# Kernel optimization log

Hardware: AMD Instinct MI355X
Metric: run time of the kernel (lower is better)

## Reference

```python
import jax, jax.numpy as jnp
import numpy as np

H = 128      # hidden_channels
FN = 6       # in_channels_node
FE = 3       # in_channels_edge
N = 40000    # nodes per chunk (pointnum)
E = 240000   # edges
C = 2        # per_t * batch_size chunks
S = 4        # n_mp_down[0] message-passing steps


def _ln(x, g, b, eps=1e-5):
    m = jnp.mean(x, axis=-1, keepdims=True)
    v = jnp.mean((x - m) ** 2, axis=-1, keepdims=True)
    return (x - m) * jax.lax.rsqrt(v + eps) * g + b


def setup_inputs() -> dict:
    key = jax.random.key(0)
    ks = iter(jax.random.split(key, 64))
    def W(*shape):
        fan_in = shape[-2]
        return jax.random.normal(next(ks), shape, jnp.float32) * (1.0 / np.sqrt(fan_in))
    z = lambda *s: jnp.zeros(s, jnp.float32)
    o = lambda *s: jnp.ones(s, jnp.float32)
    inp = {
        "x": jax.random.normal(next(ks), (C * N, FN), jnp.float32),
        "edge_attr": jax.random.normal(next(ks), (E, FE), jnp.float32),
        "mean_vec_x": jax.random.normal(next(ks), (FN,), jnp.float32) * 0.1,
        "std_vec_x": o(FN),
        "mean_vec_edge": jax.random.normal(next(ks), (FE,), jnp.float32) * 0.1,
        "std_vec_edge": o(FE),
        # node encoder: 3 linears + LayerNorm
        "nenc_w0": W(FN, H), "nenc_b0": z(H),
        "nenc_w1": W(H, H), "nenc_b1": z(H),
        "nenc_w2": W(H, H), "nenc_b2": z(H),
        "nenc_g": o(H), "nenc_be": z(H),
        # edge encoder: 3 linears + LayerNorm
        "eenc_w0": W(FE, H), "eenc_b0": z(H),
        "eenc_w1": W(H, H), "eenc_b1": z(H),
        "eenc_w2": W(H, H), "eenc_b2": z(H),
        "eenc_g": o(H), "eenc_be": z(H),
        # per-step edge MLPs (n_mlp_mp=2), stacked over S steps
        "emp_w0": W(S, 3 * H, H), "emp_b0": z(S, H),
        "emp_w1": W(S, H, H), "emp_b1": z(S, H),
        "emp_g": o(S, H), "emp_be": z(S, H),
        # per-step node MLPs
        "nmp_w0": W(S, 2 * H, H), "nmp_b0": z(S, H),
        "nmp_w1": W(S, H, H), "nmp_b1": z(S, H),
        "nmp_g": o(S, H), "nmp_be": z(S, H),
        "edge_index": jax.random.randint(next(ks), (2, E), 0, N, jnp.int32),
        "per_t": 2,
        "batch_size": 1,
    }
    return inp


def _forward(x, edge_attr, mean_vec_x, std_vec_x, mean_vec_edge, std_vec_edge,
             nenc_w0, nenc_b0, nenc_w1, nenc_b1, nenc_w2, nenc_b2, nenc_g, nenc_be,
             eenc_w0, eenc_b0, eenc_w1, eenc_b1, eenc_w2, eenc_b2, eenc_g, eenc_be,
             emp_w0, emp_b0, emp_w1, emp_b1, emp_g, emp_be,
             nmp_w0, nmp_b0, nmp_w1, nmp_b1, nmp_g, nmp_be,
             edge_index, per_t, batch_size):
    act = jax.nn.elu
    ei0, ei1 = edge_index[0], edge_index[1]
    chunks = per_t * batch_size
    n = x.shape[0] // chunks  # pointnum
    # edge encoding is identical for every chunk (shared edge_attr)
    e = (edge_attr - mean_vec_edge) / std_vec_edge
    e = act(e @ eenc_w0 + eenc_b0)
    e = act(e @ eenc_w1 + eenc_b1)
    e = e @ eenc_w2 + eenc_b2
    e0 = _ln(e, eenc_g, eenc_be)
    # scatter-mean denominator (PyG aggr='mean' at target nodes ei1)
    cnt = jax.ops.segment_sum(jnp.ones((ei1.shape[0], 1), x.dtype), ei1, num_segments=n)
    cnt = jnp.maximum(cnt, 1.0)

    def chunk(xc):  # xc: [n, FN]
        h = (xc - mean_vec_x) / std_vec_x
        h = act(h @ nenc_w0 + nenc_b0)
        h = act(h @ nenc_w1 + nenc_b1)
        h = h @ nenc_w2 + nenc_b2
        h = _ln(h, nenc_g, nenc_be)
        e = e0
        for s in range(S):
            # per-edge: gather -> concat -> 2-layer MLP -> residual -> LN
            et = jnp.concatenate([h[ei0], h[ei1], e], axis=-1)  # [E, 3H]
            et = act(et @ emp_w0[s] + emp_b0[s]) @ emp_w1[s] + emp_b1[s]
            e = _ln(e + et, emp_g[s], emp_be[s])
            # scatter-mean of edge features to target nodes
            agg = jax.ops.segment_sum(e, ei1, num_segments=n) / cnt  # [n, H]
            # per-node: concat -> 2-layer MLP -> residual -> LN
            ht = jnp.concatenate([h, agg], axis=-1)  # [n, 2H]
            ht = act(ht @ nmp_w0[s] + nmp_b0[s]) @ nmp_w1[s] + nmp_b1[s]
            h = _ln(h + ht, nmp_g[s], nmp_be[s])
        return h

    return jax.vmap(chunk)(x.reshape(chunks, n, FN))  # [C, n, H]


def reference(x, edge_attr, mean_vec_x, std_vec_x, mean_vec_edge, std_vec_edge,
              nenc_w0, nenc_b0, nenc_w1, nenc_b1, nenc_w2, nenc_b2, nenc_g, nenc_be,
              eenc_w0, eenc_b0, eenc_w1, eenc_b1, eenc_w2, eenc_b2, eenc_g, eenc_be,
              emp_w0, emp_b0, emp_w1, emp_b1, emp_g, emp_be,
              nmp_w0, nmp_b0, nmp_w1, nmp_b1, nmp_g, nmp_be,
              edge_index, per_t, batch_size):
    return _forward(x, edge_attr, mean_vec_x, std_vec_x, mean_vec_edge, std_vec_edge,
                    nenc_w0, nenc_b0, nenc_w1, nenc_b1, nenc_w2, nenc_b2, nenc_g, nenc_be,
                    eenc_w0, eenc_b0, eenc_w1, eenc_b1, eenc_w2, eenc_b2, eenc_g, eenc_be,
                    emp_w0, emp_b0, emp_w1, emp_b1, emp_g, emp_be,
                    nmp_w0, nmp_b0, nmp_w1, nmp_b1, nmp_g, nmp_be,
                    edge_index, per_t, batch_size)
```

## Files before the change

kernel.cpp:

```cpp
#include <hip/hip_runtime.h>
#include <math.h>

constexpr int HD  = 128;
constexpr int FNN = 6;
constexpr int FEE = 3;
constexpr int NN  = 40000;
constexpr int EE  = 240000;
constexpr int SS  = 4;

typedef __bf16 bf16_t;
typedef bf16_t bf16x8 __attribute__((ext_vector_type(8)));
typedef float  f32x4  __attribute__((ext_vector_type(4)));

__device__ __forceinline__ f32x4 mfma16(bf16x8 a, bf16x8 b, f32x4 c){
  return __builtin_amdgcn_mfma_f32_16x16x32_bf16(a, b, c, 0, 0, 0);
}
__device__ __forceinline__ float elu(float v){ return v > 0.f ? v : __expf(v) - 1.f; }

struct PackJob { const float* src; int K; };
struct PackArgs { PackJob j[30]; };

__global__ void __launch_bounds__(256) k_pack(PackArgs pa, bf16_t* __restrict__ dst){
  int gid = blockIdx.x*256 + threadIdx.x;
  int base = 0;
  #pragma unroll 1
  for (int i = 0; i < 30; ++i){
    int Kp = (pa.j[i].K + 31) & ~31;
    int sz = Kp * HD;
    if (gid < base + sz){
      int idx = gid - base;
      int jj = idx & 7, c = (idx >> 3) & 127, G = idx >> 10;
      int k = G*8 + jj;
      float v = (k < pa.j[i].K) ? pa.j[i].src[(size_t)k*HD + c] : 0.f;
      dst[base + idx] = (bf16_t)v;
      return;
    }
    base += sz;
  }
}

__global__ void k_cnt(const int* __restrict__ ei1, int* __restrict__ cnt){
  int t = blockIdx.x*blockDim.x + threadIdx.x;
  if (t < EE) atomicAdd(cnt + ei1[t], 1);
}

__global__ void __launch_bounds__(1024) k_scanA(const int* __restrict__ cnt,
    int* __restrict__ incl, int* __restrict__ bsum){
  __shared__ int sd[1024];
  int i = blockIdx.x*1024 + (int)threadIdx.x;
  int v = (i < NN) ? cnt[i] : 0;
  sd[threadIdx.x] = v;
  __syncthreads();
  #pragma unroll
  for (int ofs = 1; ofs < 1024; ofs <<= 1){
    int t = (threadIdx.x >= (unsigned)ofs) ? sd[threadIdx.x - ofs] : 0;
    __syncthreads();
    sd[threadIdx.x] += t;
    __syncthreads();
  }
  if (i < NN) incl[i] = sd[threadIdx.x];
  if (threadIdx.x == 1023) bsum[blockIdx.x] = sd[1023];
}
__global__ void k_scanB(const int* __restrict__ bsum, int* __restrict__ boff, int nb){
  if (threadIdx.x == 0){
    int acc = 0;
    for (int b = 0; b < nb; ++b){ boff[b] = acc; acc += bsum[b]; }
    boff[nb] = acc;
  }
}
__global__ void __launch_bounds__(1024) k_scanC(const int* __restrict__ cnt,
    const int* __restrict__ incl, const int* __restrict__ boff,
    int* __restrict__ rowstart, int* __restrict__ cursor, float* __restrict__ inv){
  int i = blockIdx.x*1024 + (int)threadIdx.x;
  if (i < NN){
    int c = cnt[i];
    int start = boff[blockIdx.x] + incl[i] - c;
    rowstart[i] = start;
    cursor[i]   = start;
    inv[i] = 1.f / fmaxf((float)c, 1.f);
  }
  if (blockIdx.x == 0 && threadIdx.x == 0) rowstart[NN] = boff[gridDim.x];
}

__global__ void k_fill(const int* __restrict__ ei0, const int* __restrict__ ei1,
                       int* __restrict__ cursor, int* __restrict__ perm,
                       int2* __restrict__ eidx2){
  int t = blockIdx.x*blockDim.x + threadIdx.x;
  if (t < EE){
    int n1 = ei1[t];
    int pos = atomicAdd(cursor + n1, 1);
    perm[pos] = t;
    int2 v; v.x = ei0[t]; v.y = n1;
    eidx2[pos] = v;
  }
}

__global__ void __launch_bounds__(256) k_agg(const bf16_t* __restrict__ e,
    const int* __restrict__ rowstart, const float* __restrict__ inv,
    bf16_t* __restrict__ agg){
  int gid = blockIdx.x*256 + (int)threadIdx.x;
  int node = gid >> 4, li = gid & 15;
  if (node >= NN) return;
  int s = rowstart[node], t = rowstart[node+1];
  float a[8] = {0,0,0,0,0,0,0,0};
  for (int ed = s; ed < t; ++ed){
    bf16x8 v = *(const bf16x8*)(e + (size_t)ed*HD + li*8);
    #pragma unroll
    for (int i = 0; i < 8; ++i) a[i] += (float)v[i];
  }
  float sc = inv[node];
  bf16x8 o;
  #pragma unroll
  for (int i = 0; i < 8; ++i) o[i] = (bf16_t)(a[i]*sc);
  *(bf16x8*)(agg + (size_t)node*HD + li*8) = o;
}

template<int FIN, bool ISNODE>
__global__ void __launch_bounds__(256) k_encoder(
    const float* __restrict__ xin, const float* __restrict__ mv, const float* __restrict__ sv,
    const float* __restrict__ w0,  const float* __restrict__ b0,
    const bf16_t* __restrict__ W1p, const float* __restrict__ b1,
    const bf16_t* __restrict__ W2p, const float* __restrict__ b2,
    const float* __restrict__ gg,  const float* __restrict__ bb,
    float* __restrict__ outf, bf16_t* __restrict__ outb,
    const int* __restrict__ perm)
{
  __shared__ bf16_t z0s[4][16][136];
  __shared__ bf16_t z1s[4][16][136];
  const int tid = threadIdx.x;
  const int w = tid >> 6, l = tid & 63, r = l & 15, grp = l >> 4;
  const int rowbase = blockIdx.x*64 + w*16;
  const int row = rowbase + r;
  const int src = perm ? perm[row] : row;

  float xn[FIN];
  #pragma unroll
  for (int f = 0; f < FIN; ++f) xn[f] = (xin[(size_t)src*FIN + f] - mv[f]) / sv[f];
  #pragma unroll
  for (int q = 0; q < 32; ++q){
    int c = grp*32 + q;
    float a = b0[c];
    #pragma unroll
    for (int f = 0; f < FIN; ++f) a += xn[f] * w0[f*HD + c];
    z0s[w][r][c] = (bf16_t)elu(a);
  }
  __syncthreads();

  bf16x8 a1[4];
  #pragma unroll
  for (int kt = 0; kt < 4; ++kt) a1[kt] = *(const bf16x8*)&z0s[w][r][kt*32 + grp*8];
  #pragma unroll
  for (int nt = 0; nt < 8; ++nt){
    int c = nt*16 + r;
    float bv = b1[c];
    f32x4 acc = {bv, bv, bv, bv};
    #pragma unroll
    for (int kt = 0; kt < 4; ++kt){
      bf16x8 bfr = *(const bf16x8*)(W1p + ((kt*4 + grp)*HD + c)*8);
      acc = mfma16(a1[kt], bfr, acc);
    }
    #pragma unroll
    for (int i = 0; i < 4; ++i) z1s[w][grp*4 + i][c] = (bf16_t)elu(acc[i]);
  }
  __syncthreads();

  bf16x8 a2[4];
  #pragma unroll
  for (int kt = 0; kt < 4; ++kt) a2[kt] = *(const bf16x8*)&z1s[w][r][kt*32 + grp*8];
  f32x4 et[8];
  #pragma unroll
  for (int nt = 0; nt < 8; ++nt){
    int c = nt*16 + r;
    float bv = b2[c];
    f32x4 acc = {bv, bv, bv, bv};
    #pragma unroll
    for (int kt = 0; kt < 4; ++kt){
      bf16x8 bfr = *(const bf16x8*)(W2p + ((kt*4 + grp)*HD + c)*8);
      acc = mfma16(a2[kt], bfr, acc);
    }
    et[nt] = acc;
  }

  f32x4 s = {0,0,0,0}, sq = {0,0,0,0};
  #pragma unroll
  for (int nt = 0; nt < 8; ++nt)
    #pragma unroll
    for (int i = 0; i < 4; ++i){ float v = et[nt][i]; s[i] += v; sq[i] += v*v; }
  #pragma unroll
  for (int m = 1; m < 16; m <<= 1)
    #pragma unroll
    for (int i = 0; i < 4; ++i){ s[i] += __shfl_xor(s[i], m, 64); sq[i] += __shfl_xor(sq[i], m, 64); }
  f32x4 mean, rstd;
  #pragma unroll
  for (int i = 0; i < 4; ++i){
    float mu = s[i] * (1.f/HD);
    float va = sq[i] * (1.f/HD) - mu*mu;
    mean[i] = mu; rstd[i] = rsqrtf(va + 1e-5f);
  }
  #pragma unroll
  for (int nt = 0; nt < 8; ++nt){
    int c = nt*16 + r;
    float gv = gg[c], bv = bb[c];
    #pragma unroll
    for (int i = 0; i < 4; ++i){
      float o = (et[nt][i] - mean[i]) * rstd[i] * gv + bv;
      size_t oidx = (size_t)(rowbase + grp*4 + i)*HD + c;
      outb[oidx] = (bf16_t)o;
      if constexpr (ISNODE) outf[oidx] = o;
    }
  }
}

__global__ void __launch_bounds__(256) k_hpartial(
    const bf16_t* __restrict__ hbf,
    const bf16_t* __restrict__ Wap, const bf16_t* __restrict__ Wbp,
    bf16_t* __restrict__ p0, bf16_t* __restrict__ p1)
{
  const int tid = threadIdx.x;
  const int w = tid >> 6, l = tid & 63, r = l & 15, grp = l >> 4;
  const int rowbase = blockIdx.x*64 + w*16;
  const int row = rowbase + r;

  bf16x8 afr[4];
  #pragma unroll
  for (int kt = 0; kt < 4; ++kt)
    afr[kt] = *(const bf16x8*)(hbf + (size_t)row*HD + kt*32 + grp*8);

  #pragma unroll
  for (int nt = 0; nt < 8; ++nt){
    int c = nt*16 + r;
    f32x4 a0 = {0,0,0,0}, a1 = {0,0,0,0};
    #pragma unroll
    for (int kt = 0; kt < 4; ++kt){
      bf16x8 bfa = *(const bf16x8*)(Wap + ((kt*4 + grp)*HD + c)*8);
      bf16x8 bfb = *(const bf16x8*)(Wbp + ((kt*4 + grp)*HD + c)*8);
      a0 = mfma16(afr[kt], bfa, a0);
      a1 = mfma16(afr[kt], bfb, a1);
    }
    #pragma unroll
    for (int i = 0; i < 4; ++i){
      size_t oidx = (size_t)(rowbase + grp*4 + i)*HD + c;
      p0[oidx] = (bf16_t)a0[i];
      p1[oidx] = (bf16_t)a1[i];
    }
  }
}

__global__ void __launch_bounds__(256) k_edge_mlp(
    const bf16_t* __restrict__ p0g, const bf16_t* __restrict__ p1g,
    const bf16_t* e_in, bf16_t* e_out,
    const bf16_t* __restrict__ W0ep, const float* __restrict__ b0,
    const bf16_t* __restrict__ W1p, const float* __restrict__ b1,
    const float* __restrict__ gg,  const float* __restrict__ bb,
    const int2* __restrict__ eidx2)
{
  __shared__ bf16_t z1s_all[4][16][136];
  const int tid = threadIdx.x;
  const int w = tid >> 6, l = tid & 63, r = l & 15, grp = l >> 4;
  const int rowbase = blockIdx.x*64 + w*16;
  const int row = rowbase + r;
  bf16_t (*z1)[136] = z1s_all[w];

  {
    const int sr = l >> 2, cq = (l & 3)*32;
    const int2 nnS = eidx2[rowbase + sr];
    const bf16_t* P0 = p0g + (size_t)nnS.x*HD + cq;
    const bf16_t* P1 = p1g + (size_t)nnS.y*HD + cq;
    #pragma unroll
    for (int q = 0; q < 4; ++q){
      bf16x8 u = *(const bf16x8*)(P0 + q*8);
      bf16x8 v = *(const bf16x8*)(P1 + q*8);
      bf16x8 sm;
      #pragma unroll
      for (int i = 0; i < 8; ++i) sm[i] = (bf16_t)((float)u[i] + (float)v[i]);
      *(bf16x8*)&z1[sr][cq + q*8] = sm;
    }
  }

  bf16x8 afr[4];
  #pragma unroll
  for (int kt = 0; kt < 4; ++kt)
    afr[kt] = *(const bf16x8*)(e_in + (size_t)row*HD + kt*32 + grp*8);
  __builtin_amdgcn_wave_barrier();

  #pragma unroll
  for (int nt = 0; nt < 8; ++nt){
    int c = nt*16 + r;
    float bv = b0[c];
    f32x4 acc = {bv, bv, bv, bv};
    #pragma unroll
    for (int kt = 0; kt < 4; ++kt){
      bf16x8 bfr = *(const bf16x8*)(W0ep + ((kt*4 + grp)*HD + c)*8);
      acc = mfma16(afr[kt], bfr, acc);
    }
    #pragma unroll
    for (int i = 0; i < 4; ++i){
      float pv = (float)z1[grp*4 + i][c];
      z1[grp*4 + i][c] = (bf16_t)elu(acc[i] + pv);
    }
  }
  __builtin_amdgcn_wave_barrier();

  bf16x8 a2[4];
  #pragma unroll
  for (int kt = 0; kt < 4; ++kt) a2[kt] = *(const bf16x8*)&z1[r][kt*32 + grp*8];
  f32x4 et[8];
  #pragma unroll
  for (int nt = 0; nt < 8; ++nt){
    int c = nt*16 + r;
    float bv = b1[c];
    f32x4 acc = {bv, bv, bv, bv};
    #pragma unroll
    for (int kt = 0; kt < 4; ++kt){
      bf16x8 bfr = *(const bf16x8*)(W1p + ((kt*4 + grp)*HD + c)*8);
      acc = mfma16(a2[kt], bfr, acc);
    }
    et[nt] = acc;
  }

  f32x4 s = {0,0,0,0}, sq = {0,0,0,0};
  #pragma unroll
  for (int nt = 0; nt < 8; ++nt){
    int c = nt*16 + r;
    #pragma unroll
    for (int i = 0; i < 4; ++i){
      float v = et[nt][i] + (float)e_in[(size_t)(rowbase + grp*4 + i)*HD + c];
      et[nt][i] = v; s[i] += v; sq[i] += v*v;
    }
  }
  #pragma unroll
  for (int m = 1; m < 16; m <<= 1)
    #pragma unroll
    for (int i = 0; i < 4; ++i){ s[i] += __shfl_xor(s[i], m, 64); sq[i] += __shfl_xor(sq[i], m, 64); }
  f32x4 mean, rstd;
  #pragma unroll
  for (int i = 0; i < 4; ++i){
    float mu = s[i] * (1.f/HD);
    float va = sq[i] * (1.f/HD) - mu*mu;
    mean[i] = mu; rstd[i] = rsqrtf(va + 1e-5f);
  }
  #pragma unroll
  for (int nt = 0; nt < 8; ++nt){
    int c = nt*16 + r;
    float gv = gg[c], bv = bb[c];
    #pragma unroll
    for (int i = 0; i < 4; ++i)
      e_out[(size_t)(rowbase + grp*4 + i)*HD + c] =
          (bf16_t)((et[nt][i] - mean[i]) * rstd[i] * gv + bv);
  }
}

template<bool DOPART>
__global__ void __launch_bounds__(256) k_node_mlp(
    bf16_t* hbf, const bf16_t* __restrict__ agg,
    const bf16_t* __restrict__ W0p, const float* __restrict__ b0,
    const bf16_t* __restrict__ W1p, const float* __restrict__ b1,
    const float* __restrict__ gg,  const float* __restrict__ bb,
    float* hout,
    const bf16_t* __restrict__ Wap, const bf16_t* __restrict__ Wbp,
    bf16_t* __restrict__ p0, bf16_t* __restrict__ p1)
{
  __shared__ bf16_t z1s[4][16][136];
  const int tid = threadIdx.x;
  const int w = tid >> 6, l = tid & 63, r = l & 15, grp = l >> 4;
  const int rowbase = blockIdx.x*64 + w*16;
  const int row = rowbase + r;

  bf16x8 afr[8];
  #pragma unroll
  for (int kt = 0; kt < 4; ++kt)
    afr[kt] = *(const bf16x8*)(hbf + (size_t)row*HD + kt*32 + grp*8);
  #pragma unroll
  for (int kt = 0; kt < 4; ++kt)
    afr[4+kt] = *(const bf16x8*)(agg + (size_t)row*HD + kt*32 + grp*8);

  #pragma unroll
  for (int nt = 0; nt < 8; ++nt){
    int c = nt*16 + r;
    float bv = b0[c];
    f32x4 acc = {bv, bv, bv, bv};
    #pragma unroll
    for (int kt = 0; kt < 8; ++kt){
      bf16x8 bfr = *(const bf16x8*)(W0p + ((kt*4 + grp)*HD + c)*8);
      acc = mfma16(afr[kt], bfr, acc);
    }
    #pragma unroll
    for (int i = 0; i < 4; ++i) z1s[w][grp*4 + i][c] = (bf16_t)elu(acc[i]);
  }
  __syncthreads();

  bf16x8 a2[4];
  #pragma unroll
  for (int kt = 0; kt < 4; ++kt) a2[kt] = *(const bf16x8*)&z1s[w][r][kt*32 + grp*8];
  f32x4 et[8];
  #pragma unroll
  for (int nt = 0; nt < 8; ++nt){
    int c = nt*16 + r;
    float bv = b1[c];
    f32x4 acc = {bv, bv, bv, bv};
    #pragma unroll
    for (int kt = 0; kt < 4; ++kt){
      bf16x8 bfr = *(const bf16x8*)(W1p + ((kt*4 + grp)*HD + c)*8);
      acc = mfma16(a2[kt], bfr, acc);
    }
    et[nt] = acc;
  }

  f32x4 s = {0,0,0,0}, sq = {0,0,0,0};
  #pragma unroll
  for (int nt = 0; nt < 8; ++nt){
    int c = nt*16 + r;
    #pragma unroll
    for (int i = 0; i < 4; ++i){
      float v = et[nt][i] + hout[(size_t)(rowbase + grp*4 + i)*HD + c];
      et[nt][i] = v; s[i] += v; sq[i] += v*v;
    }
  }
  #pragma unroll
  for (int m = 1; m < 16; m <<= 1)
    #pragma unroll
    for (int i = 0; i < 4; ++i){ s[i] += __shfl_xor(s[i], m, 64); sq[i] += __shfl_xor(sq[i], m, 64); }
  f32x4 mean, rstd;
  #pragma unroll
  for (int i = 0; i < 4; ++i){
    float mu = s[i] * (1.f/HD);
    float va = sq[i] * (1.f/HD) - mu*mu;
    mean[i] = mu; rstd[i] = rsqrtf(va + 1e-5f);
  }
  #pragma unroll
  for (int nt = 0; nt < 8; ++nt){
    int c = nt*16 + r;
    float gv = gg[c], bv = bb[c];
    #pragma unroll
    for (int i = 0; i < 4; ++i){
      float o = (et[nt][i] - mean[i]) * rstd[i] * gv + bv;
      size_t oidx = (size_t)(rowbase + grp*4 + i)*HD + c;
      bf16_t ob = (bf16_t)o;
      hout[oidx] = o;
      hbf[oidx]  = ob;
      if constexpr (DOPART) z1s[w][grp*4 + i][c] = ob;
    }
  }

  if constexpr (DOPART){
    __builtin_amdgcn_wave_barrier();
    bf16x8 ah[4];
    #pragma unroll
    for (int kt = 0; kt < 4; ++kt) ah[kt] = *(const bf16x8*)&z1s[w][r][kt*32 + grp*8];
    #pragma unroll
    for (int nt = 0; nt < 8; ++nt){
      int c = nt*16 + r;
      f32x4 a0 = {0,0,0,0}, a1 = {0,0,0,0};
      #pragma unroll
      for (int kt = 0; kt < 4; ++kt){
        bf16x8 bfa = *(const bf16x8*)(Wap + ((kt*4 + grp)*HD + c)*8);
        bf16x8 bfb = *(const bf16x8*)(Wbp + ((kt*4 + grp)*HD + c)*8);
        a0 = mfma16(ah[kt], bfa, a0);
        a1 = mfma16(ah[kt], bfb, a1);
      }
      #pragma unroll
      for (int i = 0; i < 4; ++i){
        size_t oidx = (size_t)(rowbase + grp*4 + i)*HD + c;
        p0[oidx] = (bf16_t)a0[i];
        p1[oidx] = (bf16_t)a1[i];
      }
    }
  }
}

extern "C" void kernel_launch(void* const* d_in, const int* in_sizes, int n_in,
                              void* d_out, int out_size, void* d_ws, size_t ws_size,
                              hipStream_t stream)
{
  (void)in_sizes; (void)n_in; (void)out_size; (void)ws_size;
  const float* x         = (const float*)d_in[0];
  const float* edge_attr = (const float*)d_in[1];
  const float* mvx = (const float*)d_in[2];
  const float* svx = (const float*)d_in[3];
  const float* mve = (const float*)d_in[4];
  const float* sve = (const float*)d_in[5];
  const float* nenc_w0 = (const float*)d_in[6];
  const float* nenc_b0 = (const float*)d_in[7];
  const float* nenc_w1 = (const float*)d_in[8];
  const float* nenc_b1 = (const float*)d_in[9];
  const float* nenc_w2 = (const float*)d_in[10];
  const float* nenc_b2 = (const float*)d_in[11];
  const float* nenc_g  = (const float*)d_in[12];
  const float* nenc_be = (const float*)d_in[13];
  const float* eenc_w0 = (const float*)d_in[14];
  const float* eenc_b0 = (const float*)d_in[15];
  const float* eenc_w1 = (const float*)d_in[16];
  const float* eenc_b1 = (const float*)d_in[17];
  const float* eenc_w2 = (const float*)d_in[18];
  const float* eenc_b2 = (const float*)d_in[19];
  const float* eenc_g  = (const float*)d_in[20];
  const float* eenc_be = (const float*)d_in[21];
  const float* emp_w0 = (const float*)d_in[22];
  const float* emp_b0 = (const float*)d_in[23];
  const float* emp_w1 = (const float*)d_in[24];
  const float* emp_b1 = (const float*)d_in[25];
  const float* emp_g  = (const float*)d_in[26];
  const float* emp_be = (const float*)d_in[27];
  const float* nmp_w0 = (const float*)d_in[28];
  const float* nmp_b0 = (const float*)d_in[29];
  const float* nmp_w1 = (const float*)d_in[30];
  const float* nmp_b1 = (const float*)d_in[31];
  const float* nmp_g  = (const float*)d_in[32];
  const float* nmp_be = (const float*)d_in[33];
  const int* eidx = (const int*)d_in[34];
  const int* ei0 = eidx;
  const int* ei1 = eidx + EE;
  float* out = (float*)d_out;

  char* ws = (char*)d_ws;
  size_t off = 0;
  bf16_t* e_cur = (bf16_t*)(ws + off); off += (size_t)EE*HD*2;
  bf16_t* e0    = (bf16_t*)(ws + off); off += (size_t)EE*HD*2;
  bf16_t* hbf   = (bf16_t*)(ws + off); off += (size_t)NN*HD*2;
  bf16_t* agg   = (bf16_t*)(ws + off); size_t agg_off = off; off += (size_t)NN*HD*2;
  bf16_t* p0    = (bf16_t*)(ws + off); off += (size_t)NN*HD*2;
  bf16_t* p1    = (bf16_t*)(ws + off); off += (size_t)NN*HD*2;
  float*  inv   = (float*)(ws + off);  off += (size_t)NN*4;
  int*    rowst = (int*)(ws + off);    off += (size_t)(NN+1)*4 + 12;
  int*    perm  = (int*)(ws + off);    off += (size_t)EE*4;
  int2*   eidx2 = (int2*)(ws + off);   off += (size_t)EE*8;
  bf16_t* wpk   = (bf16_t*)(ws + off);
  int*    cnt_i = (int*)(ws + agg_off);
  int*    curs  = (int*)(ws + agg_off + (size_t)NN*4);
  int*    incl  = (int*)(ws + agg_off + (size_t)2*NN*4);
  int*    bsum  = (int*)(ws + agg_off + (size_t)3*NN*4);
  int*    boff  = (int*)(ws + agg_off + (size_t)3*NN*4 + 256);

  const int NB = (NN + 1023)/1024;

  hipMemsetAsync(cnt_i, 0, NN*sizeof(int), stream);
  k_cnt<<<(EE + 255)/256, 256, 0, stream>>>(ei1, cnt_i);
  k_scanA<<<NB, 1024, 0, stream>>>(cnt_i, incl, bsum);
  k_scanB<<<1, 64, 0, stream>>>(bsum, boff, NB);
  k_scanC<<<NB, 1024, 0, stream>>>(cnt_i, incl, boff, rowst, curs, inv);
  k_fill<<<(EE + 255)/256, 256, 0, stream>>>(ei0, ei1, curs, perm, eidx2);

  PackArgs pa;
  const float* srcs[30] = {
    eenc_w0, eenc_w1, eenc_w2, nenc_w0, nenc_w1, nenc_w2,
    emp_w0,           emp_w0 + 49152,           emp_w0 + 2*49152,           emp_w0 + 3*49152,
    emp_w0 + 16384,   emp_w0 + 49152 + 16384,   emp_w0 + 2*49152 + 16384,   emp_w0 + 3*49152 + 16384,
    emp_w0 + 32768,   emp_w0 + 49152 + 32768,   emp_w0 + 2*49152 + 32768,   emp_w0 + 3*49152 + 32768,
    emp_w1, emp_w1 + 16384, emp_w1 + 2*16384, emp_w1 + 3*16384,
    nmp_w0, nmp_w0 + 32768, nmp_w0 + 2*32768, nmp_w0 + 3*32768,
    nmp_w1, nmp_w1 + 16384, nmp_w1 + 2*16384, nmp_w1 + 3*16384 };
  const int KsA[30] = {FEE,128,128,FNN,128,128,
                       128,128,128,128, 128,128,128,128, 128,128,128,128,
                       128,128,128,128, 256,256,256,256, 128,128,128,128};
  int offs[30]; int tot = 0;
  for (int i = 0; i < 30; ++i){
    pa.j[i].src = srcs[i]; pa.j[i].K = KsA[i];
    offs[i] = tot; tot += ((KsA[i] + 31) & ~31) * HD;
  }
  k_pack<<<(tot + 255)/256, 256, 0, stream>>>(pa, wpk);

  k_encoder<FEE,false><<<EE/64, 256, 0, stream>>>(edge_attr, mve, sve,
      eenc_w0, eenc_b0, wpk + offs[1], eenc_b1, wpk + offs[2], eenc_b2,
      eenc_g, eenc_be, nullptr, e0, perm);

  for (int c = 0; c < 2; ++c){
    float* hout = out + (size_t)c*NN*HD;
    k_encoder<FNN,true><<<NN/64, 256, 0, stream>>>(x + (size_t)c*NN*FNN, mvx, svx,
        nenc_w0, nenc_b0, wpk + offs[4], nenc_b1, wpk + offs[5], nenc_b2,
        nenc_g, nenc_be, hout, hbf, nullptr);
    k_hpartial<<<NN/64, 256, 0, stream>>>(hbf, wpk + offs[6], wpk + offs[10], p0, p1);
    for (int s = 0; s < SS; ++s){
      const bf16_t* e_in = (s == 0) ? e0 : e_cur;
      k_edge_mlp<<<EE/64, 256, 0, stream>>>(p0, p1, e_in, e_cur,
          wpk + offs[14+s], emp_b0 + s*HD, wpk + offs[18+s], emp_b1 + s*HD,
          emp_g + s*HD, emp_be + s*HD, eidx2);
      k_agg<<<(NN*16 + 255)/256, 256, 0, stream>>>(e_cur, rowst, inv, agg);
      if (s < SS-1){
        k_node_mlp<true><<<NN/64, 256, 0, stream>>>(hbf, agg,
            wpk + offs[22+s], nmp_b0 + s*HD, wpk + offs[26+s], nmp_b1 + s*HD,
            nmp_g + s*HD, nmp_be + s*HD, hout,
            wpk + offs[6+(s+1)], wpk + offs[10+(s+1)], p0, p1);
      } else {
        k_node_mlp<false><<<NN/64, 256, 0, stream>>>(hbf, agg,
            wpk + offs[22+s], nmp_b0 + s*HD, wpk + offs[26+s], nmp_b1 + s*HD,
            nmp_g + s*HD, nmp_be + s*HD, hout,
            nullptr, nullptr, nullptr, nullptr);
      }
    }
  }
}
```

Measured before the change: 1.082 ms.

## Batch both graph chunks into single launches per stage

```diff
diff --git a/kernel.cpp b/kernel.cpp
--- a/kernel.cpp
+++ b/kernel.cpp
@@ -7,6 +7,8 @@
 constexpr int NN  = 40000;
 constexpr int EE  = 240000;
 constexpr int SS  = 4;
+constexpr size_t NHD = (size_t)NN*HD;
+constexpr size_t EHD = (size_t)EE*HD;
 
 typedef __bf16 bf16_t;
 typedef bf16_t bf16x8 __attribute__((ext_vector_type(8)));
@@ -97,8 +99,11 @@
 
 __global__ void __launch_bounds__(256) k_agg(const bf16_t* __restrict__ e,
     const int* __restrict__ rowstart, const float* __restrict__ inv,
-    bf16_t* __restrict__ agg){
-  int gid = blockIdx.x*256 + (int)threadIdx.x;
+    bf16_t* __restrict__ agg, int nblk){
+  int bid = blockIdx.x; int c = bid / nblk; int b = bid - c*nblk;
+  e   += (size_t)c*EHD;
+  agg += (size_t)c*NHD;
+  int gid = b*256 + (int)threadIdx.x;
   int node = gid >> 4, li = gid & 15;
   if (node >= NN) return;
   int s = rowstart[node], t = rowstart[node+1];
@@ -122,14 +127,20 @@
     const bf16_t* __restrict__ W1p, const float* __restrict__ b1,
     const bf16_t* __restrict__ W2p, const float* __restrict__ b2,
     const float* __restrict__ gg,  const float* __restrict__ bb,
-    float* __restrict__ outf, bf16_t* __restrict__ outb,
-    const int* __restrict__ perm)
+    float* __restrict__ outf, bf16_t* __restrict__ outb, bf16_t* __restrict__ outb2,
+    const int* __restrict__ perm, int nblk)
 {
   __shared__ bf16_t z0s[4][16][136];
   __shared__ bf16_t z1s[4][16][136];
+  const int bid = blockIdx.x; const int c = bid / nblk; const int b = bid - c*nblk;
+  if constexpr (ISNODE){
+    xin  += (size_t)c*NN*FIN;
+    outf += (size_t)c*NHD;
+    outb += (size_t)c*NHD;
+  }
   const int tid = threadIdx.x;
   const int w = tid >> 6, l = tid & 63, r = l & 15, grp = l >> 4;
-  const int rowbase = blockIdx.x*64 + w*16;
+  const int rowbase = b*64 + w*16;
   const int row = rowbase + r;
   const int src = perm ? perm[row] : row;
 
@@ -138,11 +149,11 @@
   for (int f = 0; f < FIN; ++f) xn[f] = (xin[(size_t)src*FIN + f] - mv[f]) / sv[f];
   #pragma unroll
   for (int q = 0; q < 32; ++q){
-    int c = grp*32 + q;
-    float a = b0[c];
-    #pragma unroll
-    for (int f = 0; f < FIN; ++f) a += xn[f] * w0[f*HD + c];
-    z0s[w][r][c] = (bf16_t)elu(a);
+    int cc = grp*32 + q;
+    float a = b0[cc];
+    #pragma unroll
+    for (int f = 0; f < FIN; ++f) a += xn[f] * w0[f*HD + cc];
+    z0s[w][r][cc] = (bf16_t)elu(a);
   }
   __syncthreads();
 
@@ -151,16 +162,16 @@
   for (int kt = 0; kt < 4; ++kt) a1[kt] = *(const bf16x8*)&z0s[w][r][kt*32 + grp*8];
   #pragma unroll
   for (int nt = 0; nt < 8; ++nt){
-    int c = nt*16 + r;
-    float bv = b1[c];
+    int cc = nt*16 + r;
+    float bv = b1[cc];
     f32x4 acc = {bv, bv, bv, bv};
     #pragma unroll
     for (int kt = 0; kt < 4; ++kt){
-      bf16x8 bfr = *(const bf16x8*)(W1p + ((kt*4 + grp)*HD + c)*8);
+      bf16x8 bfr = *(const bf16x8*)(W1p + ((kt*4 + grp)*HD + cc)*8);
       acc = mfma16(a1[kt], bfr, acc);
     }
     #pragma unroll
-    for (int i = 0; i < 4; ++i) z1s[w][grp*4 + i][c] = (bf16_t)elu(acc[i]);
+    for (int i = 0; i < 4; ++i) z1s[w][grp*4 + i][cc] = (bf16_t)elu(acc[i]);
   }
   __syncthreads();
 
@@ -170,12 +181,12 @@
   f32x4 et[8];
   #pragma unroll
   for (int nt = 0; nt < 8; ++nt){
-    int c = nt*16 + r;
-    float bv = b2[c];
+    int cc = nt*16 + r;
+    float bv = b2[cc];
     f32x4 acc = {bv, bv, bv, bv};
     #pragma unroll
     for (int kt = 0; kt < 4; ++kt){
-      bf16x8 bfr = *(const bf16x8*)(W2p + ((kt*4 + grp)*HD + c)*8);
+      bf16x8 bfr = *(const bf16x8*)(W2p + ((kt*4 + grp)*HD + cc)*8);
       acc = mfma16(a2[kt], bfr, acc);
     }
     et[nt] = acc;
@@ -199,13 +210,15 @@
   }
   #pragma unroll
   for (int nt = 0; nt < 8; ++nt){
-    int c = nt*16 + r;
-    float gv = gg[c], bv = bb[c];
+    int cc = nt*16 + r;
+    float gv = gg[cc], bv = bb[cc];
     #pragma unroll
     for (int i = 0; i < 4; ++i){
       float o = (et[nt][i] - mean[i]) * rstd[i] * gv + bv;
-      size_t oidx = (size_t)(rowbase + grp*4 + i)*HD + c;
-      outb[oidx] = (bf16_t)o;
+      size_t oidx = (size_t)(rowbase + grp*4 + i)*HD + cc;
+      bf16_t ob = (bf16_t)o;
+      outb[oidx] = ob;
+      if (outb2) outb2[oidx] = ob;
       if constexpr (ISNODE) outf[oidx] = o;
     }
   }
@@ -214,11 +227,13 @@
 __global__ void __launch_bounds__(256) k_hpartial(
     const bf16_t* __restrict__ hbf,
     const bf16_t* __restrict__ Wap, const bf16_t* __restrict__ Wbp,
-    bf16_t* __restrict__ p0, bf16_t* __restrict__ p1)
+    bf16_t* __restrict__ p0, bf16_t* __restrict__ p1, int nblk)
 {
+  const int bid = blockIdx.x; const int c = bid / nblk; const int b = bid - c*nblk;
+  hbf += (size_t)c*NHD; p0 += (size_t)c*NHD; p1 += (size_t)c*NHD;
   const int tid = threadIdx.x;
   const int w = tid >> 6, l = tid & 63, r = l & 15, grp = l >> 4;
-  const int rowbase = blockIdx.x*64 + w*16;
+  const int rowbase = b*64 + w*16;
   const int row = rowbase + r;
 
   bf16x8 afr[4];
@@ -228,18 +243,18 @@
 
   #pragma unroll
   for (int nt = 0; nt < 8; ++nt){
-    int c = nt*16 + r;
+    int cc = nt*16 + r;
     f32x4 a0 = {0,0,0,0}, a1 = {0,0,0,0};
     #pragma unroll
     for (int kt = 0; kt < 4; ++kt){
-      bf16x8 bfa = *(const bf16x8*)(Wap + ((kt*4 + grp)*HD + c)*8);
-      bf16x8 bfb = *(const bf16x8*)(Wbp + ((kt*4 + grp)*HD + c)*8);
+      bf16x8 bfa = *(const bf16x8*)(Wap + ((kt*4 + grp)*HD + cc)*8);
+      bf16x8 bfb = *(const bf16x8*)(Wbp + ((kt*4 + grp)*HD + cc)*8);
       a0 = mfma16(afr[kt], bfa, a0);
       a1 = mfma16(afr[kt], bfb, a1);
     }
     #pragma unroll
     for (int i = 0; i < 4; ++i){
-      size_t oidx = (size_t)(rowbase + grp*4 + i)*HD + c;
+      size_t oidx = (size_t)(rowbase + grp*4 + i)*HD + cc;
       p0[oidx] = (bf16_t)a0[i];
       p1[oidx] = (bf16_t)a1[i];
     }
@@ -252,12 +267,15 @@
     const bf16_t* __restrict__ W0ep, const float* __restrict__ b0,
     const bf16_t* __restrict__ W1p, const float* __restrict__ b1,
     const float* __restrict__ gg,  const float* __restrict__ bb,
-    const int2* __restrict__ eidx2)
+    const int2* __restrict__ eidx2, int nblk)
 {
   __shared__ bf16_t z1s_all[4][16][136];
+  const int bid = blockIdx.x; const int c = bid / nblk; const int b = bid - c*nblk;
+  p0g += (size_t)c*NHD; p1g += (size_t)c*NHD;
+  e_in += (size_t)c*EHD; e_out += (size_t)c*EHD;
   const int tid = threadIdx.x;
   const int w = tid >> 6, l = tid & 63, r = l & 15, grp = l >> 4;
-  const int rowbase = blockIdx.x*64 + w*16;
+  const int rowbase = b*64 + w*16;
   const int row = rowbase + r;
   bf16_t (*z1)[136] = z1s_all[w];
 
@@ -285,18 +303,18 @@
 
   #pragma unroll
   for (int nt = 0; nt < 8; ++nt){
-    int c = nt*16 + r;
-    float bv = b0[c];
+    int cc = nt*16 + r;
+    float bv = b0[cc];
     f32x4 acc = {bv, bv, bv, bv};
     #pragma unroll
     for (int kt = 0; kt < 4; ++kt){
-      bf16x8 bfr = *(const bf16x8*)(W0ep + ((kt*4 + grp)*HD + c)*8);
+      bf16x8 bfr = *(const bf16x8*)(W0ep + ((kt*4 + grp)*HD + cc)*8);
       acc = mfma16(afr[kt], bfr, acc);
     }
     #pragma unroll
     for (int i = 0; i < 4; ++i){
-      float pv = (float)z1[grp*4 + i][c];
-      z1[grp*4 + i][c] = (bf16_t)elu(acc[i] + pv);
+      float pv = (float)z1[grp*4 + i][cc];
+      z1[grp*4 + i][cc] = (bf16_t)elu(acc[i] + pv);
     }
   }
   __builtin_amdgcn_wave_barrier();
@@ -307,12 +325,12 @@
   f32x4 et[8];
   #pragma unroll
   for (int nt = 0; nt < 8; ++nt){
-    int c = nt*16 + r;
-    float bv = b1[c];
+    int cc = nt*16 + r;
+    float bv = b1[cc];
     f32x4 acc = {bv, bv, bv, bv};
     #pragma unroll
     for (int kt = 0; kt < 4; ++kt){
-      bf16x8 bfr = *(const bf16x8*)(W1p + ((kt*4 + grp)*HD + c)*8);
+      bf16x8 bfr = *(const bf16x8*)(W1p + ((kt*4 + grp)*HD + cc)*8);
       acc = mfma16(a2[kt], bfr, acc);
     }
     et[nt] = acc;
@@ -321,10 +339,10 @@
   f32x4 s = {0,0,0,0}, sq = {0,0,0,0};
   #pragma unroll
   for (int nt = 0; nt < 8; ++nt){
-    int c = nt*16 + r;
+    int cc = nt*16 + r;
     #pragma unroll
     for (int i = 0; i < 4; ++i){
-      float v = et[nt][i] + (float)e_in[(size_t)(rowbase + grp*4 + i)*HD + c];
+      float v = et[nt][i] + (float)e_in[(size_t)(rowbase + grp*4 + i)*HD + cc];
       et[nt][i] = v; s[i] += v; sq[i] += v*v;
     }
   }
@@ -341,11 +359,11 @@
   }
   #pragma unroll
   for (int nt = 0; nt < 8; ++nt){
-    int c = nt*16 + r;
-    float gv = gg[c], bv = bb[c];
+    int cc = nt*16 + r;
+    float gv = gg[cc], bv = bb[cc];
     #pragma unroll
     for (int i = 0; i < 4; ++i)
-      e_out[(size_t)(rowbase + grp*4 + i)*HD + c] =
+      e_out[(size_t)(rowbase + grp*4 + i)*HD + cc] =
           (bf16_t)((et[nt][i] - mean[i]) * rstd[i] * gv + bv);
   }
 }
@@ -358,12 +376,15 @@
     const float* __restrict__ gg,  const float* __restrict__ bb,
     float* hout,
     const bf16_t* __restrict__ Wap, const bf16_t* __restrict__ Wbp,
-    bf16_t* __restrict__ p0, bf16_t* __restrict__ p1)
+    bf16_t* __restrict__ p0, bf16_t* __restrict__ p1, int nblk)
 {
   __shared__ bf16_t z1s[4][16][136];
+  const int bid = blockIdx.x; const int c = bid / nblk; const int b = bid - c*nblk;
+  hbf += (size_t)c*NHD; agg += (size_t)c*NHD; hout += (size_t)c*NHD;
+  if constexpr (DOPART){ p0 += (size_t)c*NHD; p1 += (size_t)c*NHD; }
   const int tid = threadIdx.x;
   const int w = tid >> 6, l = tid & 63, r = l & 15, grp = l >> 4;
-  const int rowbase = blockIdx.x*64 + w*16;
+  const int rowbase = b*64 + w*16;
   const int row = rowbase + r;
 
   bf16x8 afr[8];
@@ -376,16 +397,16 @@
 
   #pragma unroll
   for (int nt = 0; nt < 8; ++nt){
-    int c = nt*16 + r;
-    float bv = b0[c];
+    int cc = nt*16 + r;
+    float bv = b0[cc];
     f32x4 acc = {bv, bv, bv, bv};
     #pragma unroll
     for (int kt = 0; kt < 8; ++kt){
-      bf16x8 bfr = *(const bf16x8*)(W0p + ((kt*4 + grp)*HD + c)*8);
+      bf16x8 bfr = *(const bf16x8*)(W0p + ((kt*4 + grp)*HD + cc)*8);
       acc = mfma16(afr[kt], bfr, acc);
     }
     #pragma unroll
-    for (int i = 0; i < 4; ++i) z1s[w][grp*4 + i][c] = (bf16_t)elu(acc[i]);
+    for (int i = 0; i < 4; ++i) z1s[w][grp*4 + i][cc] = (bf16_t)elu(acc[i]);
   }
   __syncthreads();
 
@@ -395,12 +416,12 @@
   f32x4 et[8];
   #pragma unroll
   for (int nt = 0; nt < 8; ++nt){
-    int c = nt*16 + r;
-    float bv = b1[c];
+    int cc = nt*16 + r;
+    float bv = b1[cc];
     f32x4 acc = {bv, bv, bv, bv};
     #pragma unroll
     for (int kt = 0; kt < 4; ++kt){
-      bf16x8 bfr = *(const bf16x8*)(W1p + ((kt*4 + grp)*HD + c)*8);
+      bf16x8 bfr = *(const bf16x8*)(W1p + ((kt*4 + grp)*HD + cc)*8);
       acc = mfma16(a2[kt], bfr, acc);
     }
     et[nt] = acc;
@@ -409,10 +430,10 @@
   f32x4 s = {0,0,0,0}, sq = {0,0,0,0};
   #pragma unroll
   for (int nt = 0; nt < 8; ++nt){
-    int c = nt*16 + r;
+    int cc = nt*16 + r;
     #pragma unroll
     for (int i = 0; i < 4; ++i){
-      float v = et[nt][i] + hout[(size_t)(rowbase + grp*4 + i)*HD + c];
+      float v = et[nt][i] + hout[(size_t)(rowbase + grp*4 + i)*HD + cc];
       et[nt][i] = v; s[i] += v; sq[i] += v*v;
     }
   }
@@ -429,16 +450,16 @@
   }
   #pragma unroll
   for (int nt = 0; nt < 8; ++nt){
-    int c = nt*16 + r;
-    float gv = gg[c], bv = bb[c];
+    int cc = nt*16 + r;
+    float gv = gg[cc], bv = bb[cc];
     #pragma unroll
     for (int i = 0; i < 4; ++i){
       float o = (et[nt][i] - mean[i]) * rstd[i] * gv + bv;
-      size_t oidx = (size_t)(rowbase + grp*4 + i)*HD + c;
+      size_t oidx = (size_t)(rowbase + grp*4 + i)*HD + cc;
       bf16_t ob = (bf16_t)o;
       hout[oidx] = o;
       hbf[oidx]  = ob;
-      if constexpr (DOPART) z1s[w][grp*4 + i][c] = ob;
+      if constexpr (DOPART) z1s[w][grp*4 + i][cc] = ob;
     }
   }
 
@@ -449,18 +470,18 @@
     for (int kt = 0; kt < 4; ++kt) ah[kt] = *(const bf16x8*)&z1s[w][r][kt*32 + grp*8];
     #pragma unroll
     for (int nt = 0; nt < 8; ++nt){
-      int c = nt*16 + r;
+      int cc = nt*16 + r;
       f32x4 a0 = {0,0,0,0}, a1 = {0,0,0,0};
       #pragma unroll
       for (int kt = 0; kt < 4; ++kt){
-        bf16x8 bfa = *(const bf16x8*)(Wap + ((kt*4 + grp)*HD + c)*8);
-        bf16x8 bfb = *(const bf16x8*)(Wbp + ((kt*4 + grp)*HD + c)*8);
+        bf16x8 bfa = *(const bf16x8*)(Wap + ((kt*4 + grp)*HD + cc)*8);
+        bf16x8 bfb = *(const bf16x8*)(Wbp + ((kt*4 + grp)*HD + cc)*8);
         a0 = mfma16(ah[kt], bfa, a0);
         a1 = mfma16(ah[kt], bfb, a1);
       }
       #pragma unroll
       for (int i = 0; i < 4; ++i){
-        size_t oidx = (size_t)(rowbase + grp*4 + i)*HD + c;
+        size_t oidx = (size_t)(rowbase + grp*4 + i)*HD + cc;
         p0[oidx] = (bf16_t)a0[i];
         p1[oidx] = (bf16_t)a1[i];
       }
@@ -472,7 +493,7 @@
                               void* d_out, int out_size, void* d_ws, size_t ws_size,
                               hipStream_t stream)
 {
-  (void)in_sizes; (void)n_in; (void)out_size; (void)ws_size;
+  (void)in_sizes; (void)n_in; (void)out_size;
   const float* x         = (const float*)d_in[0];
   const float* edge_attr = (const float*)d_in[1];
   const float* mvx = (const float*)d_in[2];
@@ -512,34 +533,6 @@
   const int* ei1 = eidx + EE;
   float* out = (float*)d_out;
 
-  char* ws = (char*)d_ws;
-  size_t off = 0;
-  bf16_t* e_cur = (bf16_t*)(ws + off); off += (size_t)EE*HD*2;
-  bf16_t* e0    = (bf16_t*)(ws + off); off += (size_t)EE*HD*2;
-  bf16_t* hbf   = (bf16_t*)(ws + off); off += (size_t)NN*HD*2;
-  bf16_t* agg   = (bf16_t*)(ws + off); size_t agg_off = off; off += (size_t)NN*HD*2;
-  bf16_t* p0    = (bf16_t*)(ws + off); off += (size_t)NN*HD*2;
-  bf16_t* p1    = (bf16_t*)(ws + off); off += (size_t)NN*HD*2;
-  float*  inv   = (float*)(ws + off);  off += (size_t)NN*4;
-  int*    rowst = (int*)(ws + off);    off += (size_t)(NN+1)*4 + 12;
-  int*    perm  = (int*)(ws + off);    off += (size_t)EE*4;
-  int2*   eidx2 = (int2*)(ws + off);   off += (size_t)EE*8;
-  bf16_t* wpk   = (bf16_t*)(ws + off);
-  int*    cnt_i = (int*)(ws + agg_off);
-  int*    curs  = (int*)(ws + agg_off + (size_t)NN*4);
-  int*    incl  = (int*)(ws + agg_off + (size_t)2*NN*4);
-  int*    bsum  = (int*)(ws + agg_off + (size_t)3*NN*4);
-  int*    boff  = (int*)(ws + agg_off + (size_t)3*NN*4 + 256);
-
-  const int NB = (NN + 1023)/1024;
-
-  hipMemsetAsync(cnt_i, 0, NN*sizeof(int), stream);
-  k_cnt<<<(EE + 255)/256, 256, 0, stream>>>(ei1, cnt_i);
-  k_scanA<<<NB, 1024, 0, stream>>>(cnt_i, incl, bsum);
-  k_scanB<<<1, 64, 0, stream>>>(bsum, boff, NB);
-  k_scanC<<<NB, 1024, 0, stream>>>(cnt_i, incl, boff, rowst, curs, inv);
-  k_fill<<<(EE + 255)/256, 256, 0, stream>>>(ei0, ei1, curs, perm, eidx2);
-
   PackArgs pa;
   const float* srcs[30] = {
     eenc_w0, eenc_w1, eenc_w2, nenc_w0, nenc_w1, nenc_w2,
@@ -557,35 +550,123 @@
     pa.j[i].src = srcs[i]; pa.j[i].K = KsA[i];
     offs[i] = tot; tot += ((KsA[i] + 31) & ~31) * HD;
   }
-  k_pack<<<(tot + 255)/256, 256, 0, stream>>>(pa, wpk);
-
-  k_encoder<FEE,false><<<EE/64, 256, 0, stream>>>(edge_attr, mve, sve,
-      eenc_w0, eenc_b0, wpk + offs[1], eenc_b1, wpk + offs[2], eenc_b2,
-      eenc_g, eenc_be, nullptr, e0, perm);
-
-  for (int c = 0; c < 2; ++c){
-    float* hout = out + (size_t)c*NN*HD;
-    k_encoder<FNN,true><<<NN/64, 256, 0, stream>>>(x + (size_t)c*NN*FNN, mvx, svx,
+
+  const int NBn = NN/64;
+  const int NBe = EE/64;
+  const int NBa = (NN*16 + 255)/256;
+  const int NB  = (NN + 1023)/1024;
+
+  size_t need_merged = 2*EHD*2 + 8*NHD*2 + (size_t)NN*4 + (size_t)(NN+1)*4 + 64
+                     + (size_t)EE*4 + (size_t)EE*8 + (size_t)tot*2 + 1024;
+
+  char* ws = (char*)d_ws;
+
+  if (ws_size >= need_merged){
+    size_t off = 0;
+    bf16_t* e_cur = (bf16_t*)(ws + off); off += 2*EHD*2;
+    bf16_t* hbf   = (bf16_t*)(ws + off); off += 2*NHD*2;
+    bf16_t* agg   = (bf16_t*)(ws + off); size_t agg_off = off; off += 2*NHD*2;
+    bf16_t* p0    = (bf16_t*)(ws + off); off += 2*NHD*2;
+    bf16_t* p1    = (bf16_t*)(ws + off); off += 2*NHD*2;
+    float*  inv   = (float*)(ws + off);  off += (size_t)NN*4;
+    int*    rowst = (int*)(ws + off);    off += (size_t)(NN+1)*4 + 12;
+    int*    perm  = (int*)(ws + off);    off += (size_t)EE*4;
+    int2*   eidx2 = (int2*)(ws + off);   off += (size_t)EE*8;
+    bf16_t* wpk   = (bf16_t*)(ws + off);
+    int*    cnt_i = (int*)(ws + agg_off);
+    int*    curs  = (int*)(ws + agg_off + (size_t)NN*4);
+    int*    incl  = (int*)(ws + agg_off + (size_t)2*NN*4);
+    int*    bsum  = (int*)(ws + agg_off + (size_t)3*NN*4);
+    int*    boff  = (int*)(ws + agg_off + (size_t)3*NN*4 + 256);
+
+    hipMemsetAsync(cnt_i, 0, NN*sizeof(int), stream);
+    k_cnt<<<(EE + 255)/256, 256, 0, stream>>>(ei1, cnt_i);
+    k_scanA<<<NB, 1024, 0, stream>>>(cnt_i, incl, bsum);
+    k_scanB<<<1, 64, 0, stream>>>(bsum, boff, NB);
+    k_scanC<<<NB, 1024, 0, stream>>>(cnt_i, incl, boff, rowst, curs, inv);
+    k_fill<<<(EE + 255)/256, 256, 0, stream>>>(ei0, ei1, curs, perm, eidx2);
+    k_pack<<<(tot + 255)/256, 256, 0, stream>>>(pa, wpk);
+
+    k_encoder<FEE,false><<<NBe, 256, 0, stream>>>(edge_attr, mve, sve,
+        eenc_w0, eenc_b0, wpk + offs[1], eenc_b1, wpk + offs[2], eenc_b2,
+        eenc_g, eenc_be, nullptr, e_cur, e_cur + EHD, perm, NBe);
+    k_encoder<FNN,true><<<2*NBn, 256, 0, stream>>>(x, mvx, svx,
         nenc_w0, nenc_b0, wpk + offs[4], nenc_b1, wpk + offs[5], nenc_b2,
-        nenc_g, nenc_be, hout, hbf, nullptr);
-    k_hpartial<<<NN/64, 256, 0, stream>>>(hbf, wpk + offs[6], wpk + offs[10], p0, p1);
+        nenc_g, nenc_be, out, hbf, nullptr, nullptr, NBn);
+    k_hpartial<<<2*NBn, 256, 0, stream>>>(hbf, wpk + offs[6], wpk + offs[10], p0, p1, NBn);
+
     for (int s = 0; s < SS; ++s){
-      const bf16_t* e_in = (s == 0) ? e0 : e_cur;
-      k_edge_mlp<<<EE/64, 256, 0, stream>>>(p0, p1, e_in, e_cur,
+      k_edge_mlp<<<2*NBe, 256, 0, stream>>>(p0, p1, e_cur, e_cur,
           wpk + offs[14+s], emp_b0 + s*HD, wpk + offs[18+s], emp_b1 + s*HD,
-          emp_g + s*HD, emp_be + s*HD, eidx2);
-      k_agg<<<(NN*16 + 255)/256, 256, 0, stream>>>(e_cur, rowst, inv, agg);
+          emp_g + s*HD, emp_be + s*HD, eidx2, NBe);
+      k_agg<<<2*NBa, 256, 0, stream>>>(e_cur, rowst, inv, agg, NBa);
       if (s < SS-1){
-        k_node_mlp<true><<<NN/64, 256, 0, stream>>>(hbf, agg,
+        k_node_mlp<true><<<2*NBn, 256, 0, stream>>>(hbf, agg,
             wpk + offs[22+s], nmp_b0 + s*HD, wpk + offs[26+s], nmp_b1 + s*HD,
-            nmp_g + s*HD, nmp_be + s*HD, hout,
-            wpk + offs[6+(s+1)], wpk + offs[10+(s+1)], p0, p1);
+            nmp_g + s*HD, nmp_be + s*HD, out,
+            wpk + offs[6+(s+1)], wpk + offs[10+(s+1)], p0, p1, NBn);
       } else {
-        k_node_mlp<false><<<NN/64, 256, 0, stream>>>(hbf, agg,
+        k_node_mlp<false><<<2*NBn, 256, 0, stream>>>(hbf, agg,
             wpk + offs[22+s], nmp_b0 + s*HD, wpk + offs[26+s], nmp_b1 + s*HD,
-            nmp_g + s*HD, nmp_be + s*HD, hout,
-            nullptr, nullptr, nullptr, nullptr);
+            nmp_g + s*HD, nmp_be + s*HD, out,
+            nullptr, nullptr, nullptr, nullptr, NBn);
       }
     }
-  }
-}
+  } else {
+    size_t off = 0;
+    bf16_t* e_cur = (bf16_t*)(ws + off); off += EHD*2;
+    bf16_t* e0    = (bf16_t*)(ws + off); off += EHD*2;
+    bf16_t* hbf   = (bf16_t*)(ws + off); off += NHD*2;
+    bf16_t* agg   = (bf16_t*)(ws + off); size_t agg_off = off; off += NHD*2;
+    bf16_t* p0    = (bf16_t*)(ws + off); off += NHD*2;
+    bf16_t* p1    = (bf16_t*)(ws + off); off += NHD*2;
+    float*  inv   = (float*)(ws + off);  off += (size_t)NN*4;
+    int*    rowst = (int*)(ws + off);    off += (size_t)(NN+1)*4 + 12;
+    int*    perm  = (int*)(ws + off);    off += (size_t)EE*4;
+    int2*   eidx2 = (int2*)(ws + off);   off += (size_t)EE*8;
+    bf16_t* wpk   = (bf16_t*)(ws + off);
+    int*    cnt_i = (int*)(ws + agg_off);
+    int*    curs  = (int*)(ws + agg_off + (size_t)NN*4);
+    int*    incl  = (int*)(ws + agg_off + (size_t)2*NN*4);
+    int*    bsum  = (int*)(ws + agg_off + (size_t)3*NN*4);
+    int*    boff  = (int*)(ws + agg_off + (size_t)3*NN*4 + 256);
+
+    hipMemsetAsync(cnt_i, 0, NN*sizeof(int), stream);
+    k_cnt<<<(EE + 255)/256, 256, 0, stream>>>(ei1, cnt_i);
+    k_scanA<<<NB, 1024, 0, stream>>>(cnt_i, incl, bsum);
+    k_scanB<<<1, 64, 0, stream>>>(bsum, boff, NB);
+    k_scanC<<<NB, 1024, 0, stream>>>(cnt_i, incl, boff, rowst, curs, inv);
+    k_fill<<<(EE + 255)/256, 256, 0, stream>>>(ei0, ei1, curs, perm, eidx2);
+    k_pack<<<(tot + 255)/256, 256, 0, stream>>>(pa, wpk);
+
+    k_encoder<FEE,false><<<NBe, 256, 0, stream>>>(edge_attr, mve, sve,
+        eenc_w0, eenc_b0, wpk + offs[1], eenc_b1, wpk + offs[2], eenc_b2,
+        eenc_g, eenc_be, nullptr, e0, nullptr, perm, NBe);
+
+    for (int c = 0; c < 2; ++c){
+      float* hout = out + (size_t)c*NHD;
+      k_encoder<FNN,true><<<NBn, 256, 0, stream>>>(x + (size_t)c*NN*FNN, mvx, svx,
+          nenc_w0, nenc_b0, wpk + offs[4], nenc_b1, wpk + offs[5], nenc_b2,
+          nenc_g, nenc_be, hout, hbf, nullptr, nullptr, NBn);
+      k_hpartial<<<NBn, 256, 0, stream>>>(hbf, wpk + offs[6], wpk + offs[10], p0, p1, NBn);
+      for (int s = 0; s < SS; ++s){
+        const bf16_t* e_in = (s == 0) ? e0 : e_cur;
+        k_edge_mlp<<<NBe, 256, 0, stream>>>(p0, p1, e_in, e_cur,
+            wpk + offs[14+s], emp_b0 + s*HD, wpk + offs[18+s], emp_b1 + s*HD,
+            emp_g + s*HD, emp_be + s*HD, eidx2, NBe);
+        k_agg<<<NBa, 256, 0, stream>>>(e_cur, rowst, inv, agg, NBa);
+        if (s < SS-1){
+          k_node_mlp<true><<<NBn, 256, 0, stream>>>(hbf, agg,
+              wpk + offs[22+s], nmp_b0 + s*HD, wpk + offs[26+s], nmp_b1 + s*HD,
+              nmp_g + s*HD, nmp_be + s*HD, hout,
+              wpk + offs[6+(s+1)], wpk + offs[10+(s+1)], p0, p1, NBn);
+        } else {
+          k_node_mlp<false><<<NBn, 256, 0, stream>>>(hbf, agg,
+              wpk + offs[22+s], nmp_b0 + s*HD, wpk + offs[26+s], nmp_b1 + s*HD,
+              nmp_g + s*HD, nmp_be + s*HD, hout,
+              nullptr, nullptr, nullptr, nullptr, NBn);
+        }
+      }
+    }
+  }
+}
```

Measured after the change: 984.0 us. 1.1x faster.
